# Kernel optimization log

Hardware: AMD Instinct MI355X
Metric: run time of the kernel (lower is better)

Reference implementation:

```python
import jax, jax.numpy as jnp
import numpy as np
from jax import lax

N_BLOCKS = 5
POOL = 15
N_HEADS = 8
LATENT = 32
N_EXPERTS = 4


def setup_inputs() -> dict:
    key = jax.random.key(0)
    ks = jax.random.split(key, 24)
    B, T, D = 4, 2048, 512
    H = 2 * D  # expert_dim
    s = 0.02
    f = lambda k, shp: (jax.random.normal(k, shp, jnp.float32) * s)
    return {
        'x': jax.random.normal(ks[0], (B, T, D), jnp.float32),
        # TemporalGating gate_proj
        'tg_w': f(ks[1], (D, N_BLOCKS)), 'tg_b': jnp.zeros((N_BLOCKS,), jnp.float32),
        # DualScaleFusion
        'mp_w': f(ks[2], (D, D)), 'mp_b': jnp.zeros((D,), jnp.float32),
        'fu_w': f(ks[3], (2 * D, D)), 'fu_b': jnp.zeros((D,), jnp.float32),
        # MLAAttention (all no-bias)
        'wc': f(ks[4], (D, LATENT)), 'wk': f(ks[5], (LATENT, D)),
        'wv': f(ks[6], (LATENT, D)), 'wq': f(ks[7], (D, D)), 'wo': f(ks[8], (D, D)),
        # RMSNorms
        's1': jnp.ones((D,), jnp.float32), 's2': jnp.ones((D,), jnp.float32),
        # GatedMoE
        'wr': f(ks[9], (D, N_EXPERTS)), 'br': jnp.zeros((N_EXPERTS,), jnp.float32),
        'wg': f(ks[10], (D, D)), 'bg': jnp.zeros((D,), jnp.float32),
        'w1': f(ks[11], (N_EXPERTS, D, H)), 'b1': jnp.zeros((N_EXPERTS, H), jnp.float32),
        'w2': f(ks[12], (N_EXPERTS, H, D)), 'b2': jnp.zeros((N_EXPERTS, D), jnp.float32),
    }


def _temporal_gate(x, tg_w, tg_b):
    B, T, D = x.shape
    bs = T // N_BLOCKS
    tl = N_BLOCKS * bs
    r = x[:, :tl].reshape(B, N_BLOCKS, bs, D)          # [B,nb,bs,D]
    bm = r.mean(axis=2)                                 # [B,nb,D]
    imp = jax.nn.softmax(bm @ tg_w + tg_b, axis=-1)     # [B,nb,nb]
    imp = imp.mean(axis=-1, keepdims=True)              # [B,nb,1]
    g = (r * imp[..., None]).reshape(B, tl, D)
    return jnp.pad(g, ((0, 0), (0, T - tl), (0, 0)))


def _dual_scale(x, mp_w, mp_b, fu_w, fu_b):
    # AveragePooling1D(pool=15, stride=1, SAME): TF excludes padding from the mean.
    B, T, D = x.shape
    sums = lax.reduce_window(x, 0.0, lax.add, (1, POOL, 1), (1, 1, 1), 'SAME')
    cnt = lax.reduce_window(jnp.ones((1, T, 1), x.dtype), 0.0, lax.add,
                            (1, POOL, 1), (1, 1, 1), 'SAME')
    macro = sums / cnt
    macro_feat = macro @ mp_w + mp_b
    return jnp.concatenate([x, macro_feat], axis=-1) @ fu_w + fu_b


def _mla_attn(x, wc, wk, wv, wq, wo):
    B, T, D = x.shape
    dh = D // N_HEADS
    split = lambda t: t.reshape(B, T, N_HEADS, dh).transpose(0, 2, 1, 3)
    latent = x @ wc                                      # [B,T,L]
    K, V, Q = split(latent @ wk), split(latent @ wv), split(x @ wq)
    scores = jnp.einsum('bhqd,bhkd->bhqk', Q, K) / jnp.sqrt(jnp.float32(dh))
    causal = jnp.tril(jnp.ones((T, T), jnp.float32))
    scores = scores + (1.0 - causal) * -1e9
    attn = jax.nn.softmax(scores, axis=-1)
    out = jnp.einsum('bhqk,bhkd->bhqd', attn, V).transpose(0, 2, 1, 3).reshape(B, T, D)
    return out @ wo


def _rmsnorm(x, scale, eps=1e-6):
    var = jnp.mean(jnp.square(x), axis=-1, keepdims=True)
    return scale * (x * lax.rsqrt(var + eps))


def _moe(x, wr, br, wg, bg, w1, b1, w2, b2):
    w = jax.nn.softmax(x @ wr + br, axis=-1)             # [B,T,E]
    xg = x * jax.nn.sigmoid(x @ wg + bg)
    h = jax.nn.gelu(jnp.einsum('btd,edh->bteh', xg, w1) + b1, approximate=False)
    eo = jnp.einsum('bteh,ehd->bted', h, w2) + b2        # [B,T,E,D]
    return jnp.einsum('bted,bte->btd', eo, w)


def reference(x, tg_w, tg_b, mp_w, mp_b, fu_w, fu_b, wc, wk, wv, wq, wo,
              s1, s2, wr, br, wg, bg, w1, b1, w2, b2):
    xf = _temporal_gate(x, tg_w, tg_b)
    xfu = _dual_scale(xf, mp_w, mp_b, fu_w, fu_b)
    x1 = _rmsnorm(x + _mla_attn(xfu, wc, wk, wv, wq, wo), s1)
    return _rmsnorm(x1 + _moe(x1, wr, br, wg, bg, w1, b1, w2, b2), s2)
```

## Files before the change

### kernel.cpp

```cpp
#include <hip/hip_runtime.h>
#include <math.h>

#define B_   4
#define T_   2048
#define D_   512
#define TOK  (B_*T_)
#define TL_  2045
#define GATE 0.2f
#define QSCALE 0.18033688011112043f

typedef unsigned short u16;
typedef __attribute__((ext_vector_type(8))) short short8;
typedef __attribute__((ext_vector_type(4))) float f32x4;

static __device__ __forceinline__ u16 f2u(float f){
    union { float f; unsigned u; } a; a.f = f;
    unsigned r = a.u + 0x7fffu + ((a.u >> 16) & 1u);
    return (u16)(r >> 16);
}
static __device__ __forceinline__ float u2f(u16 u){
    union { unsigned u; float f; } a; a.u = ((unsigned)u) << 16;
    return a.f;
}
static __device__ __forceinline__ f32x4 mfma16(short8 a, short8 b, f32x4 c){
    return __builtin_amdgcn_mfma_f32_16x16x32_bf16(a, b, c, 0, 0, 0);
}
static __device__ __forceinline__ void glds16(const u16* g, u16* l){
    __builtin_amdgcn_global_load_lds((const __attribute__((address_space(1))) void*)g,
                                     (__attribute__((address_space(3))) void*)l, 16, 0, 0);
}

__global__ __launch_bounds__(256) void gatepool_kernel(
    const float* __restrict__ x, u16* __restrict__ xfcat)
{
    int idx = blockIdx.x*256 + threadIdx.x;
    int d = idx & 511, g = idx >> 9;
    int b = g >> 7, t0 = (g & 127) << 4;
    const float* xp = x + ((size_t)b*2048)*512 + d;
    float v[30];
    #pragma unroll
    for (int j = 0; j < 30; ++j){
        int u = t0 - 7 + j;
        v[j] = (u >= 0 && u < TL_) ? xp[(size_t)u*512] : 0.f;
    }
    float p[31]; p[0] = 0.f;
    #pragma unroll
    for (int j = 0; j < 30; ++j) p[j+1] = p[j] + v[j];
    u16* xc = xfcat + ((size_t)(b*2048 + t0))*1024 + d;
    #pragma unroll
    for (int i = 0; i < 16; ++i){
        int t = t0 + i;
        float sum = p[i+15] - p[i];
        int lo = t-7; if (lo < 0) lo = 0;
        int hi = t+7; if (hi > 2047) hi = 2047;
        xc[(size_t)i*1024]       = f2u((t < TL_) ? GATE*v[i+7] : 0.f);
        xc[(size_t)i*1024 + 512] = f2u(GATE * sum / (float)(hi - lo + 1));
    }
}

struct TJob { const float* src; u16* dst; int K, N, ldout, coloff, tiles; float scale; };
struct TJobs { TJob j[13]; int n; };

__global__ __launch_bounds__(256) void tconv_all_kernel(TJobs JJ){
    __shared__ float t[32][33];
    int idx = blockIdx.x;
    int jb = 0;
    while (jb < JJ.n - 1 && idx >= JJ.j[jb].tiles){ idx -= JJ.j[jb].tiles; ++jb; }
    TJob J = JJ.j[jb];
    int tX = J.N >> 5;
    int k0 = (idx / tX) * 32, n0 = (idx % tX) * 32;
    int tx = threadIdx.x & 31, ty = threadIdx.x >> 5;
    #pragma unroll
    for (int i = 0; i < 32; i += 8)
        t[ty+i][tx] = J.src[(size_t)(k0+ty+i)*J.N + n0+tx];
    __syncthreads();
    #pragma unroll
    for (int i = 0; i < 32; i += 8)
        J.dst[(size_t)(n0+ty+i)*J.ldout + J.coloff + k0+tx] = f2u(J.scale * t[tx][ty+i]);
}

__global__ void convert_kernel(const float* __restrict__ in, u16* __restrict__ out){
    int idx = blockIdx.x*256 + threadIdx.x;
    out[idx] = f2u(in[idx]);
}

__global__ __launch_bounds__(256) void biasfold_kernel(
    const float* __restrict__ fu_b, const float* __restrict__ mp_b,
    const float* __restrict__ fu_w, float* __restrict__ out)
{
    int n = blockIdx.x, tid = threadIdx.x;
    float s = mp_b[tid]*fu_w[(size_t)(512+tid)*512 + n]
            + mp_b[tid+256]*fu_w[(size_t)(768+tid)*512 + n];
    for (int off = 32; off; off >>= 1) s += __shfl_down(s, off);
    __shared__ float ws[4];
    if ((tid & 63) == 0) ws[tid >> 6] = s;
    __syncthreads();
    if (tid == 0) out[n] = fu_b[n] + ws[0]+ws[1]+ws[2]+ws[3];
}

__global__ __launch_bounds__(256) void sgemm_kernel(const float* __restrict__ A,
    const float* __restrict__ B, u16* __restrict__ dstT, float* __restrict__ outF, int K){
    __shared__ float As[16][65];
    __shared__ float Bs[16][65];
    int tid = threadIdx.x;
    int tx = tid & 15, ty = tid >> 4;
    int m0 = blockIdx.y*64, n0 = blockIdx.x*64;
    int arow = tid >> 2, akq = (tid & 3) * 4;
    int bk = tid >> 4, bn = (tid & 15) * 4;
    float acc[4][4] = {};
    for (int k0 = 0; k0 < K; k0 += 16){
        const float* Ap = A + (size_t)(m0+arow)*K + k0 + akq;
        As[akq+0][arow]=Ap[0]; As[akq+1][arow]=Ap[1];
        As[akq+2][arow]=Ap[2]; As[akq+3][arow]=Ap[3];
        const float* Bp = B + (size_t)(k0+bk)*512 + n0 + bn;
        Bs[bk][bn+0]=Bp[0]; Bs[bk][bn+1]=Bp[1];
        Bs[bk][bn+2]=Bp[2]; Bs[bk][bn+3]=Bp[3];
        __syncthreads();
        #pragma unroll
        for (int kk = 0; kk < 16; ++kk){
            float av[4], bv[4];
            #pragma unroll
            for (int i=0;i<4;++i) av[i]=As[kk][ty*4+i];
            #pragma unroll
            for (int j=0;j<4;++j) bv[j]=Bs[kk][tx*4+j];
            #pragma unroll
            for (int i=0;i<4;++i)
                #pragma unroll
                for (int j=0;j<4;++j) acc[i][j] += av[i]*bv[j];
        }
        __syncthreads();
    }
    if (outF){
        #pragma unroll
        for (int i=0;i<4;++i)
            #pragma unroll
            for (int j=0;j<4;++j)
                outF[(size_t)(m0+ty*4+i)*512 + n0+tx*4+j] = acc[i][j];
    } else {
        #pragma unroll
        for (int i=0;i<4;++i)
            #pragma unroll
            for (int j=0;j<4;++j)
                dstT[(size_t)(n0+tx*4+j)*512 + m0+ty*4+i] = f2u(acc[i][j]);
    }
}

#define GF_GELU   1
#define GF_ACCUM  2
#define GF_RSCOL  4
#define GF_GLU    8
#define GF_F32OUT 16
#define GF_QKV    32

template<int MT>
__global__ __launch_bounds__(256) void mgemm_kernel(
    const u16* __restrict__ A, int lda, const u16* __restrict__ Bt, int ldb,
    const float* __restrict__ bias, const float* __restrict__ rs,
    const u16* __restrict__ glu, void* __restrict__ Cp, int ldc,
    u16* __restrict__ Cp2, int K, int flags)
{
    constexpr int MI = MT/32;
    __shared__ u16 As[MT*64];
    __shared__ u16 Bs[128*64];
    int tid = threadIdx.x;
    int wave = tid >> 6, lane = tid & 63;
    int n16 = lane & 15, quad = lane >> 4;
    int m0 = blockIdx.y * MT, n0 = blockIdx.x * 128;
    int wr = (wave >> 1) * (MT/2), wc = (wave & 1) * 64;

    f32x4 acc[MI][4] = {};

    for (int k0 = 0; k0 < K; k0 += 64){
        #pragma unroll
        for (int i = 0; i < MT/32; ++i){
            int s = i*256 + tid;
            int row = s >> 3, g = (s & 7) ^ (row & 7);
            glds16(A + (size_t)(m0+row)*lda + k0 + g*8, As + (size_t)s*8);
        }
        #pragma unroll
        for (int i = 0; i < 4; ++i){
            int s = i*256 + tid;
            int row = s >> 3, g = (s & 7) ^ (row & 7);
            glds16(Bt + (size_t)(n0+row)*ldb + k0 + g*8, Bs + (size_t)s*8);
        }
        __syncthreads();
        #pragma unroll
        for (int ks = 0; ks < 2; ++ks){
            short8 af[MI], bf[4];
            #pragma unroll
            for (int mi = 0; mi < MI; ++mi){
                int row = wr + mi*16 + n16;
                int g = (ks*4 + quad) ^ (row & 7);
                af[mi] = *(const short8*)&As[row*64 + g*8];
            }
            #pragma unroll
            for (int ni = 0; ni < 4; ++ni){
                int row = wc + ni*16 + n16;
                int g = (ks*4 + quad) ^ (row & 7);
                bf[ni] = *(const short8*)&Bs[row*64 + g*8];
            }
            #pragma unroll
            for (int mi = 0; mi < MI; ++mi)
                #pragma unroll
                for (int ni = 0; ni < 4; ++ni)
                    acc[mi][ni] = mfma16(af[mi], bf[ni], acc[mi][ni]);
        }
        __syncthreads();
    }

    if ((flags & GF_QKV) && n0 >= 1024){
        #pragma unroll
        for (int mi = 0; mi < MI; ++mi){
            int row0 = m0 + wr + mi*16 + quad*4;
            #pragma unroll
            for (int ni = 0; ni < 4; ++ni){
                int col = n0 + wc + ni*16 + n16 - 1024;
                ushort4 h4;
                h4.x = f2u(acc[mi][ni][0]); h4.y = f2u(acc[mi][ni][1]);
                h4.z = f2u(acc[mi][ni][2]); h4.w = f2u(acc[mi][ni][3]);
                *(ushort4*)&Cp2[(size_t)col*8192 + row0] = h4;
            }
        }
        return;
    }

    #pragma unroll
    for (int mi = 0; mi < MI; ++mi){
        #pragma unroll
        for (int reg = 0; reg < 4; ++reg){
            int row = m0 + wr + mi*16 + quad*4 + reg;
            #pragma unroll
            for (int ni = 0; ni < 4; ++ni){
                int col = n0 + wc + ni*16 + n16;
                float v = acc[mi][ni][reg];
                if (bias) v += bias[col];
                if (flags & GF_GELU)  v = 0.5f*v*(1.f + erff(v*0.70710678118f));
                if (flags & GF_GLU)   v = u2f(glu[(size_t)row*512 + col]) / (1.f + __expf(-v));
                if (flags & GF_RSCOL) v *= rs[(size_t)row*4 + (col >> 10)];
                size_t ci = (size_t)row*ldc + col;
                if (flags & GF_ACCUM)       ((float*)Cp)[ci] += v;
                else if (flags & GF_F32OUT) ((float*)Cp)[ci]  = v;
                else                        ((u16*)Cp)[ci]    = f2u(v);
            }
        }
    }
}

__global__ __launch_bounds__(256) void flash_kernel(
    const u16* __restrict__ QK,
    const u16* __restrict__ VT,
    u16* __restrict__ O)
{
    int bid = blockIdx.x;
    int qt = 15 - (bid >> 5);
    int bh = bid & 31;
    int h = bh & 7, b = bh >> 3;
    __shared__ u16 Ks[64*64];
    __shared__ u16 Vt[64*64];
    __shared__ u16 Ps[4][32*64];
    int tid = threadIdx.x;
    int wave = tid >> 6, lane = tid & 63;
    int n16 = lane & 15, quad = lane >> 4;
    size_t btok = (size_t)b*2048;
    size_t tok0 = btok + qt*128;

    short8 qf[2][2];
    #pragma unroll
    for (int g = 0; g < 2; ++g)
        #pragma unroll
        for (int ks = 0; ks < 2; ++ks)
            qf[g][ks] = *(const short8*)&QK[(tok0 + wave*32 + g*16 + n16)*1024
                                           + h*64 + ks*32 + quad*8];

    int qlo[2];  qlo[0] = qt*128 + wave*32; qlo[1] = qlo[0] + 16;
    int qrow[2]; qrow[0] = qlo[0] + n16;    qrow[1] = qlo[1] + n16;
    float m_st[2] = {-3.0e38f, -3.0e38f}, l_st[2] = {0.f, 0.f};
    f32x4 ov[2][4] = {};

    int nkt = 2*qt + 2;
    for (int kt = 0; kt < nkt; ++kt){
        __syncthreads();
        {
            int r = tid >> 2;
            int g0 = (tid & 3) * 2;
            const uint4* kp = (const uint4*)&QK[(btok + kt*64 + r)*1024 + 512 + h*64 + g0*8];
            uint4 ka = kp[0], kb = kp[1];
            *(uint4*)&Ks[r*64 + ((g0  ) ^ (r&7))*8] = ka;
            *(uint4*)&Ks[r*64 + ((g0+1) ^ (r&7))*8] = kb;
            const uint4* vp = (const uint4*)&VT[(size_t)(h*64 + r)*8192 + btok + kt*64 + g0*8];
            uint4 va = vp[0], vb = vp[1];
            *(uint4*)&Vt[r*64 + ((g0  ) ^ (r&7))*8] = va;
            *(uint4*)&Vt[r*64 + ((g0+1) ^ (r&7))*8] = vb;
        }
        __syncthreads();

        bool act[2];
        #pragma unroll
        for (int g = 0; g < 2; ++g){
            act[g] = (kt*64 <= qlo[g] + 15);
            if (!act[g]) continue;
            f32x4 st[4];
            #pragma unroll
            for (int ct = 0; ct < 4; ++ct){
                f32x4 a = {};
                #pragma unroll
                for (int ks = 0; ks < 2; ++ks){
                    short8 kf = *(const short8*)&Ks[(ct*16+n16)*64 + (((ks*4+quad) ^ (n16&7))*8)];
                    a = mfma16(kf, qf[g][ks], a);
                }
                st[ct] = a;
            }
            if (kt*64 + 63 > qlo[g]){
                #pragma unroll
                for (int ct = 0; ct < 4; ++ct){
                    int kb0 = kt*64 + ct*16 + quad*4;
                    #pragma unroll
                    for (int r = 0; r < 4; ++r)
                        if (kb0 + r > qrow[g]) st[ct][r] = -3.0e38f;
                }
            }
            float mx = fmaxf(fmaxf(fmaxf(st[0][0],st[0][1]),fmaxf(st[0][2],st[0][3])),
                       fmaxf(fmaxf(fmaxf(st[1][0],st[1][1]),fmaxf(st[1][2],st[1][3])),
                       fmaxf(fmaxf(fmaxf(st[2][0],st[2][1]),fmaxf(st[2][2],st[2][3])),
                             fmaxf(fmaxf(st[3][0],st[3][1]),fmaxf(st[3][2],st[3][3])))));
            mx = fmaxf(mx, __shfl_xor(mx, 16));
            mx = fmaxf(mx, __shfl_xor(mx, 32));
            float mn = fmaxf(m_st[g], mx);
            float al = exp2f(m_st[g] - mn);
            m_st[g] = mn;
            float sum = 0.f;
            #pragma unroll
            for (int ct = 0; ct < 4; ++ct)
                #pragma unroll
                for (int r = 0; r < 4; ++r){
                    float p = exp2f(st[ct][r] - mn);
                    st[ct][r] = p; sum += p;
                }
            sum += __shfl_xor(sum, 16);
            sum += __shfl_xor(sum, 32);
            l_st[g] = l_st[g]*al + sum;
            int qr = g*16 + n16;
            #pragma unroll
            for (int ct = 0; ct < 4; ++ct){
                ushort4 h4;
                h4.x = f2u(st[ct][0]); h4.y = f2u(st[ct][1]);
                h4.z = f2u(st[ct][2]); h4.w = f2u(st[ct][3]);
                int goff = ct*2 + (quad >> 1);
                *(ushort4*)&Ps[wave][qr*64 + ((goff ^ (qr&7))*8) + (quad&1)*4] = h4;
            }
            #pragma unroll
            for (int r = 0; r < 4; ++r){
                float aa = __shfl(al, quad*4 + r);
                #pragma unroll
                for (int dt = 0; dt < 4; ++dt) ov[g][dt][r] *= aa;
            }
        }
        #pragma unroll
        for (int g = 0; g < 2; ++g){
            if (!act[g]) continue;
            short8 ap[2];
            int row = g*16 + n16;
            #pragma unroll
            for (int ks = 0; ks < 2; ++ks)
                ap[ks] = *(const short8*)&Ps[wave][row*64 + (((ks*4+quad) ^ (row&7))*8)];
            #pragma unroll
            for (int dt = 0; dt < 4; ++dt)
                #pragma unroll
                for (int ks = 0; ks < 2; ++ks){
                    short8 bv = *(const short8*)&Vt[(dt*16+n16)*64 + (((ks*4+quad) ^ (n16&7))*8)];
                    ov[g][dt] = mfma16(ap[ks], bv, ov[g][dt]);
                }
        }
    }
    #pragma unroll
    for (int g = 0; g < 2; ++g)
        #pragma unroll
        for (int r = 0; r < 4; ++r){
            float li = __shfl(l_st[g], quad*4 + r);
            float inv = 1.f / li;
            size_t row = tok0 + wave*32 + g*16 + quad*4 + r;
            #pragma unroll
            for (int dt = 0; dt < 4; ++dt)
                O[row*512 + h*64 + dt*16 + n16] = f2u(ov[g][dt][r] * inv);
        }
}

__global__ __launch_bounds__(256) void rmsnorm_kernel(
    const float* __restrict__ x, const u16* __restrict__ y,
    const float* __restrict__ scale, u16* __restrict__ out)
{
    int tok = blockIdx.x, tid = threadIdx.x;
    size_t base = (size_t)tok * 512;
    float v0 = x[base+tid]     + u2f(y[base+tid]);
    float v1 = x[base+tid+256] + u2f(y[base+tid+256]);
    float ss = v0*v0 + v1*v1;
    for (int off = 32; off; off >>= 1) ss += __shfl_down(ss, off);
    __shared__ float ws[4];
    if ((tid & 63) == 0) ws[tid >> 6] = ss;
    __syncthreads();
    float rstd = rsqrtf((ws[0]+ws[1]+ws[2]+ws[3])*(1.f/512.f) + 1e-6f);
    out[base+tid]     = f2u(scale[tid]     * v0 * rstd);
    out[base+tid+256] = f2u(scale[tid+256] * v1 * rstd);
}

__global__ __launch_bounds__(256) void final_kernel(
    const u16* __restrict__ x1, const float* __restrict__ moe,
    const float* __restrict__ rout, const float* __restrict__ b2,
    const float* __restrict__ scale, float* __restrict__ out)
{
    int tok = blockIdx.x, tid = threadIdx.x;
    size_t base = (size_t)tok * 512;
    float r0 = rout[tok*4+0], r1 = rout[tok*4+1], r2 = rout[tok*4+2], r3 = rout[tok*4+3];
    float bb0 = r0*b2[tid]     + r1*b2[512+tid]     + r2*b2[1024+tid]     + r3*b2[1536+tid];
    float bb1 = r0*b2[tid+256] + r1*b2[768+tid]     + r2*b2[1280+tid]     + r3*b2[1792+tid];
    float v0 = u2f(x1[base+tid])     + moe[base+tid]     + bb0;
    float v1 = u2f(x1[base+tid+256]) + moe[base+tid+256] + bb1;
    float ss = v0*v0 + v1*v1;
    for (int off = 32; off; off >>= 1) ss += __shfl_down(ss, off);
    __shared__ float ws[4];
    if ((tid & 63) == 0) ws[tid >> 6] = ss;
    __syncthreads();
    float rstd = rsqrtf((ws[0]+ws[1]+ws[2]+ws[3])*(1.f/512.f) + 1e-6f);
    out[base+tid]     = scale[tid]     * v0 * rstd;
    out[base+tid+256] = scale[tid+256] * v1 * rstd;
}

__global__ __launch_bounds__(256) void router_kernel(
    const u16* __restrict__ x1, const float* __restrict__ wr,
    const float* __restrict__ br, float* __restrict__ rout)
{
    int wid = threadIdx.x >> 6, lane = threadIdx.x & 63;
    int tok = blockIdx.x*4 + wid;
    const u16* xp = x1 + (size_t)tok*512;
    float p0=0.f, p1=0.f, p2=0.f, p3=0.f;
    for (int d = lane; d < 512; d += 64){
        float xv = u2f(xp[d]);
        p0 += xv*wr[d*4+0]; p1 += xv*wr[d*4+1];
        p2 += xv*wr[d*4+2]; p3 += xv*wr[d*4+3];
    }
    for (int off = 32; off; off >>= 1){
        p0 += __shfl_down(p0,off); p1 += __shfl_down(p1,off);
        p2 += __shfl_down(p2,off); p3 += __shfl_down(p3,off);
    }
    if (lane == 0){
        p0 += br[0]; p1 += br[1]; p2 += br[2]; p3 += br[3];
        float mx = fmaxf(fmaxf(p0,p1), fmaxf(p2,p3));
        float e0=__expf(p0-mx), e1=__expf(p1-mx), e2=__expf(p2-mx), e3=__expf(p3-mx);
        float inv = 1.f/(e0+e1+e2+e3);
        rout[tok*4+0]=e0*inv; rout[tok*4+1]=e1*inv;
        rout[tok*4+2]=e2*inv; rout[tok*4+3]=e3*inv;
    }
}

extern "C" void kernel_launch(void* const* d_in, const int* in_sizes, int n_in,
                              void* d_out, int out_size, void* d_ws, size_t ws_size,
                              hipStream_t stream)
{
    const float* x    = (const float*)d_in[0];
    const float* mp_w = (const float*)d_in[3];
    const float* mp_b = (const float*)d_in[4];
    const float* fu_w = (const float*)d_in[5];
    const float* fu_b = (const float*)d_in[6];
    const float* wc   = (const float*)d_in[7];
    const float* wk   = (const float*)d_in[8];
    const float* wv   = (const float*)d_in[9];
    const float* wq   = (const float*)d_in[10];
    const float* wo   = (const float*)d_in[11];
    const float* s1   = (const float*)d_in[12];
    const float* s2   = (const float*)d_in[13];
    const float* wr   = (const float*)d_in[14];
    const float* br   = (const float*)d_in[15];
    const float* wg   = (const float*)d_in[16];
    const float* bg   = (const float*)d_in[17];
    const float* w1   = (const float*)d_in[18];
    const float* b1   = (const float*)d_in[19];
    const float* w2   = (const float*)d_in[20];
    const float* b2   = (const float*)d_in[21];

    char* wsb = (char*)d_ws;
    const size_t MB = 1024*1024;
    const size_t KB512 = 512*1024;
    u16*   wqkvT  = (u16*)(wsb + 0);
    u16*   woT    = (u16*)(wsb + 3*KB512);
    u16*   wgT    = (u16*)(wsb + 4*KB512);
    u16*   WfuT2  = (u16*)(wsb + 5*KB512);
    u16*   fuBT   = (u16*)(wsb + 7*KB512);
    u16*   mp_wB  = (u16*)(wsb + 8*KB512);
    u16*   w1T    = (u16*)(wsb + 9*KB512);
    u16*   w2Ts   = (u16*)(wsb + 17*KB512);
    float* WcvF   = (float*)(wsb + 25*KB512);
    float* fubias = (float*)(wsb + 27*KB512);
    float* ROUT   = (float*)(wsb + 27*KB512 + 4096);
    u16*   XFcat = (u16*)(wsb + 14*MB);
    float* MOE   = (float*)(wsb + 14*MB);
    u16*   S3    = (u16*)(wsb + 14*MB);
    u16*   XFU   = (u16*)(wsb + 30*MB);
    u16*   XG    = (u16*)(wsb + 30*MB);
    u16*   QKb   = (u16*)(wsb + 38*MB);
    u16*   Hb    = (u16*)(wsb + 38*MB);
    u16*   ATT   = (u16*)(wsb + 54*MB);
    u16*   VbT   = (u16*)(wsb + 70*MB);
    u16*   x1h   = (u16*)(wsb + 78*MB);

    auto mg128 = [&](const u16* A, int lda, const u16* Bt, int ldb, const float* bias,
                     const float* rs, const u16* glu, void* C, int ldc, u16* C2,
                     int M, int N, int K, int flags){
        dim3 g(N/128, M/128);
        mgemm_kernel<128><<<g, 256, 0, stream>>>(A, lda, Bt, ldb, bias, rs, glu, C, ldc, C2, K, flags);
    };
    auto mg64 = [&](const u16* A, int lda, const u16* Bt, int ldb, const float* bias,
                    const float* rs, const u16* glu, void* C, int ldc, u16* C2,
                    int M, int N, int K, int flags){
        dim3 g(N/128, M/64);
        mgemm_kernel<64><<<g, 256, 0, stream>>>(A, lda, Bt, ldb, bias, rs, glu, C, ldc, C2, K, flags);
    };

    TJobs JJ; JJ.n = 13;
    auto setj = [&](int i, const float* src, u16* dst, int K, int N, int ldout,
                    int coloff, float scale){
        JJ.j[i] = TJob{src, dst, K, N, ldout, coloff, (K/32)*(N/32), scale};
    };
    setj(0, wq,            wqkvT, 512,  512,  512, 0, QSCALE);
    setj(1, wo,            woT,   512,  512,  512, 0, 1.f);
    setj(2, wg,            wgT,   512,  512,  512, 0, 1.f);
    setj(3, fu_w,          WfuT2, 512,  512, 1024, 0, 1.f);
    setj(4, fu_w + 512*512,fuBT,  512,  512,  512, 0, 1.f);
    for (int e = 0; e < 4; ++e){
        setj(5+e, w1 + (size_t)e*512*1024, w1T + (size_t)e*1024*512, 512, 1024, 512, 0, 1.f);
        setj(9+e, w2 + (size_t)e*1024*512, w2Ts + (size_t)e*1024, 1024, 512, 4096, 0, 1.f);
    }
    int nt = 5*256 + 4*512 + 4*512;
    tconv_all_kernel<<<nt, 256, 0, stream>>>(JJ);
    convert_kernel<<<512*512/256, 256, 0, stream>>>(mp_w, mp_wB);
    sgemm_kernel<<<dim3(8,8), 256, 0, stream>>>(wc, wk, wqkvT + 512*512, nullptr, 32);
    sgemm_kernel<<<dim3(8,8), 256, 0, stream>>>(wc, wv, wqkvT + 1024*512, nullptr, 32);
    biasfold_kernel<<<512, 256, 0, stream>>>(fu_b, mp_b, fu_w, fubias);
    mg64(fuBT, 512, mp_wB, 512, 0, 0, 0, WfuT2 + 512, 1024, 0, 512, 512, 512, 0);
    (void)WcvF;

    gatepool_kernel<<<(TOK/16)*512/256, 256, 0, stream>>>(x, XFcat);
    mg64 (XFcat, 1024, WfuT2, 1024, fubias, 0, 0, XFU, 512, 0, TOK, 512, 1024, 0);
    mg64 (XFU, 512, wqkvT, 512, 0, 0, 0, QKb, 1024, VbT, TOK, 1536, 512, GF_QKV);
    flash_kernel<<<512, 256, 0, stream>>>(QKb, VbT, ATT);
    mg64 (ATT, 512, woT, 512, 0, 0, 0, S3, 512, 0, TOK, 512, 512, 0);
    rmsnorm_kernel<<<TOK, 256, 0, stream>>>(x, S3, s1, x1h);
    router_kernel<<<TOK/4, 256, 0, stream>>>(x1h, wr, br, ROUT);
    mg64 (x1h, 512, wgT, 512, bg, 0, x1h, XG, 512, 0, TOK, 512, 512, GF_GLU);
    for (int p = 0; p < 2; ++p){
        mg128(XG, 512, w1T + (size_t)p*2048*512, 512, b1 + p*2048, ROUT + p*2, 0,
              Hb, 2048, 0, TOK, 2048, 512, GF_GELU | GF_RSCOL);
        mg64 (Hb, 2048, w2Ts + p*2048, 4096, 0, 0, 0,
              MOE, 512, 0, TOK, 512, 2048, p ? GF_ACCUM : GF_F32OUT);
    }
    final_kernel<<<TOK, 256, 0, stream>>>(x1h, MOE, ROUT, b2, s2, (float*)d_out);
}
```

Before: 588.2 us.

## Fold fusion GEMM into QKV weights and split MoE by token halves

Measured after the change: 612.9 us. +4.2%, slower.

```diff
diff --git a/kernel.cpp b/kernel.cpp
--- a/kernel.cpp
+++ b/kernel.cpp
@@ -98,8 +98,22 @@
     if (tid == 0) out[n] = fu_b[n] + ws[0]+ws[1]+ws[2]+ws[3];
 }
 
+__global__ __launch_bounds__(256) void qkvbias_kernel(
+    const float* __restrict__ fubias, const u16* __restrict__ wqkvT,
+    float* __restrict__ out)
+{
+    int n = blockIdx.x, tid = threadIdx.x;
+    const u16* wp = wqkvT + (size_t)n*512;
+    float s = fubias[tid]*u2f(wp[tid]) + fubias[tid+256]*u2f(wp[tid+256]);
+    for (int off = 32; off; off >>= 1) s += __shfl_down(s, off);
+    __shared__ float ws[4];
+    if ((tid & 63) == 0) ws[tid >> 6] = s;
+    __syncthreads();
+    if (tid == 0) out[n] = ws[0]+ws[1]+ws[2]+ws[3];
+}
+
 __global__ __launch_bounds__(256) void sgemm_kernel(const float* __restrict__ A,
-    const float* __restrict__ B, u16* __restrict__ dstT, float* __restrict__ outF, int K){
+    const float* __restrict__ B, u16* __restrict__ dstT, int K){
     __shared__ float As[16][65];
     __shared__ float Bs[16][65];
     int tid = threadIdx.x;
@@ -130,26 +144,16 @@
         }
         __syncthreads();
     }
-    if (outF){
-        #pragma unroll
-        for (int i=0;i<4;++i)
-            #pragma unroll
-            for (int j=0;j<4;++j)
-                outF[(size_t)(m0+ty*4+i)*512 + n0+tx*4+j] = acc[i][j];
-    } else {
-        #pragma unroll
-        for (int i=0;i<4;++i)
-            #pragma unroll
-            for (int j=0;j<4;++j)
-                dstT[(size_t)(n0+tx*4+j)*512 + m0+ty*4+i] = f2u(acc[i][j]);
-    }
+    #pragma unroll
+    for (int i=0;i<4;++i)
+        #pragma unroll
+        for (int j=0;j<4;++j)
+            dstT[(size_t)(n0+tx*4+j)*512 + m0+ty*4+i] = f2u(acc[i][j]);
 }
 
 #define GF_GELU   1
-#define GF_ACCUM  2
 #define GF_RSCOL  4
 #define GF_GLU    8
-#define GF_F32OUT 16
 #define GF_QKV    32
 
 template<int MT>
@@ -214,11 +218,12 @@
             int row0 = m0 + wr + mi*16 + quad*4;
             #pragma unroll
             for (int ni = 0; ni < 4; ++ni){
-                int col = n0 + wc + ni*16 + n16 - 1024;
+                int col = n0 + wc + ni*16 + n16;
+                float bb = bias[col];
                 ushort4 h4;
-                h4.x = f2u(acc[mi][ni][0]); h4.y = f2u(acc[mi][ni][1]);
-                h4.z = f2u(acc[mi][ni][2]); h4.w = f2u(acc[mi][ni][3]);
-                *(ushort4*)&Cp2[(size_t)col*8192 + row0] = h4;
+                h4.x = f2u(acc[mi][ni][0] + bb); h4.y = f2u(acc[mi][ni][1] + bb);
+                h4.z = f2u(acc[mi][ni][2] + bb); h4.w = f2u(acc[mi][ni][3] + bb);
+                *(ushort4*)&Cp2[(size_t)(col-1024)*8192 + row0] = h4;
             }
         }
         return;
@@ -237,10 +242,7 @@
                 if (flags & GF_GELU)  v = 0.5f*v*(1.f + erff(v*0.70710678118f));
                 if (flags & GF_GLU)   v = u2f(glu[(size_t)row*512 + col]) / (1.f + __expf(-v));
                 if (flags & GF_RSCOL) v *= rs[(size_t)row*4 + (col >> 10)];
-                size_t ci = (size_t)row*ldc + col;
-                if (flags & GF_ACCUM)       ((float*)Cp)[ci] += v;
-                else if (flags & GF_F32OUT) ((float*)Cp)[ci]  = v;
-                else                        ((u16*)Cp)[ci]    = f2u(v);
+                ((u16*)Cp)[(size_t)row*ldc + col] = f2u(v);
             }
         }
     }
@@ -404,7 +406,7 @@
 }
 
 __global__ __launch_bounds__(256) void final_kernel(
-    const u16* __restrict__ x1, const float* __restrict__ moe,
+    const u16* __restrict__ x1, const u16* __restrict__ moe,
     const float* __restrict__ rout, const float* __restrict__ b2,
     const float* __restrict__ scale, float* __restrict__ out)
 {
@@ -413,8 +415,8 @@
     float r0 = rout[tok*4+0], r1 = rout[tok*4+1], r2 = rout[tok*4+2], r3 = rout[tok*4+3];
     float bb0 = r0*b2[tid]     + r1*b2[512+tid]     + r2*b2[1024+tid]     + r3*b2[1536+tid];
     float bb1 = r0*b2[tid+256] + r1*b2[768+tid]     + r2*b2[1280+tid]     + r3*b2[1792+tid];
-    float v0 = u2f(x1[base+tid])     + moe[base+tid]     + bb0;
-    float v1 = u2f(x1[base+tid+256]) + moe[base+tid+256] + bb1;
+    float v0 = u2f(x1[base+tid])     + u2f(moe[base+tid])     + bb0;
+    float v1 = u2f(x1[base+tid+256]) + u2f(moe[base+tid+256]) + bb1;
     float ss = v0*v0 + v1*v1;
     for (int off = 32; off; off >>= 1) ss += __shfl_down(ss, off);
     __shared__ float ws[4];
@@ -479,28 +481,27 @@
 
     char* wsb = (char*)d_ws;
     const size_t MB = 1024*1024;
-    const size_t KB512 = 512*1024;
-    u16*   wqkvT  = (u16*)(wsb + 0);
-    u16*   woT    = (u16*)(wsb + 3*KB512);
-    u16*   wgT    = (u16*)(wsb + 4*KB512);
-    u16*   WfuT2  = (u16*)(wsb + 5*KB512);
-    u16*   fuBT   = (u16*)(wsb + 7*KB512);
-    u16*   mp_wB  = (u16*)(wsb + 8*KB512);
-    u16*   w1T    = (u16*)(wsb + 9*KB512);
-    u16*   w2Ts   = (u16*)(wsb + 17*KB512);
-    float* WcvF   = (float*)(wsb + 25*KB512);
-    float* fubias = (float*)(wsb + 27*KB512);
-    float* ROUT   = (float*)(wsb + 27*KB512 + 4096);
-    u16*   XFcat = (u16*)(wsb + 14*MB);
-    float* MOE   = (float*)(wsb + 14*MB);
-    u16*   S3    = (u16*)(wsb + 14*MB);
-    u16*   XFU   = (u16*)(wsb + 30*MB);
-    u16*   XG    = (u16*)(wsb + 30*MB);
-    u16*   QKb   = (u16*)(wsb + 38*MB);
-    u16*   Hb    = (u16*)(wsb + 38*MB);
-    u16*   ATT   = (u16*)(wsb + 54*MB);
-    u16*   VbT   = (u16*)(wsb + 70*MB);
-    u16*   x1h   = (u16*)(wsb + 78*MB);
+    u16*   WqkvC  = (u16*)(wsb + 0);
+    u16*   woT    = (u16*)(wsb + 3*MB);
+    u16*   wgT    = (u16*)(wsb + 3*MB + 512*1024);
+    u16*   w1T    = (u16*)(wsb + 4*MB);
+    u16*   w2Ts   = (u16*)(wsb + 8*MB);
+    float* fubias = (float*)(wsb + 12*MB);
+    float* qkvbias= (float*)(wsb + 12*MB + 4096);
+    float* ROUT   = (float*)(wsb + 12*MB + 16384);
+    u16*   wqkvT  = (u16*)(wsb + 25*MB/2);
+    u16*   fuBT   = (u16*)(wsb + 14*MB);
+    u16*   mp_wB  = (u16*)(wsb + 29*MB/2);
+    u16*   WfuBF  = (u16*)(wsb + 15*MB);
+    u16*   XFcat = (u16*)(wsb + 16*MB);
+    u16*   S3    = (u16*)(wsb + 16*MB);
+    u16*   MOE   = (u16*)(wsb + 16*MB);
+    u16*   x1h   = (u16*)(wsb + 24*MB);
+    u16*   QKb   = (u16*)(wsb + 32*MB);
+    u16*   XG    = (u16*)(wsb + 32*MB);
+    u16*   Hb    = (u16*)(wsb + 40*MB);
+    u16*   VbT   = (u16*)(wsb + 48*MB);
+    u16*   ATT   = (u16*)(wsb + 56*MB);
 
     auto mg128 = [&](const u16* A, int lda, const u16* Bt, int ldb, const float* bias,
                      const float* rs, const u16* glu, void* C, int ldc, u16* C2,
@@ -515,7 +516,7 @@
         mgemm_kernel<64><<<g, 256, 0, stream>>>(A, lda, Bt, ldb, bias, rs, glu, C, ldc, C2, K, flags);
     };
 
-    TJobs JJ; JJ.n = 13;
+    TJobs JJ; JJ.n = 11;
     auto setj = [&](int i, const float* src, u16* dst, int K, int N, int ldout,
                     int coloff, float scale){
         JJ.j[i] = TJob{src, dst, K, N, ldout, coloff, (K/32)*(N/32), scale};
@@ -523,34 +524,34 @@
     setj(0, wq,            wqkvT, 512,  512,  512, 0, QSCALE);
     setj(1, wo,            woT,   512,  512,  512, 0, 1.f);
     setj(2, wg,            wgT,   512,  512,  512, 0, 1.f);
-    setj(3, fu_w,          WfuT2, 512,  512, 1024, 0, 1.f);
-    setj(4, fu_w + 512*512,fuBT,  512,  512,  512, 0, 1.f);
+    setj(3, fu_w + 512*512,fuBT,  512,  512,  512, 0, 1.f);
     for (int e = 0; e < 4; ++e){
-        setj(5+e, w1 + (size_t)e*512*1024, w1T + (size_t)e*1024*512, 512, 1024, 512, 0, 1.f);
-        setj(9+e, w2 + (size_t)e*1024*512, w2Ts + (size_t)e*1024, 1024, 512, 4096, 0, 1.f);
-    }
-    int nt = 5*256 + 4*512 + 4*512;
+        setj(4+e, w1 + (size_t)e*512*1024, w1T + (size_t)e*1024*512, 512, 1024, 512, 0, 1.f);
+        setj(8+e, w2 + (size_t)e*1024*512, w2Ts + (size_t)e*1024, 1024, 512, 4096, 0, 1.f);
+    }
+    int nt = 4*256 + 8*512;
     tconv_all_kernel<<<nt, 256, 0, stream>>>(JJ);
     convert_kernel<<<512*512/256, 256, 0, stream>>>(mp_w, mp_wB);
-    sgemm_kernel<<<dim3(8,8), 256, 0, stream>>>(wc, wk, wqkvT + 512*512, nullptr, 32);
-    sgemm_kernel<<<dim3(8,8), 256, 0, stream>>>(wc, wv, wqkvT + 1024*512, nullptr, 32);
+    convert_kernel<<<512*512/256, 256, 0, stream>>>(fu_w, WfuBF);
+    sgemm_kernel<<<dim3(8,8), 256, 0, stream>>>(wc, wk, wqkvT + 512*512, 32);
+    sgemm_kernel<<<dim3(8,8), 256, 0, stream>>>(wc, wv, wqkvT + 1024*512, 32);
     biasfold_kernel<<<512, 256, 0, stream>>>(fu_b, mp_b, fu_w, fubias);
-    mg64(fuBT, 512, mp_wB, 512, 0, 0, 0, WfuT2 + 512, 1024, 0, 512, 512, 512, 0);
-    (void)WcvF;
+    qkvbias_kernel<<<1536, 256, 0, stream>>>(fubias, wqkvT, qkvbias);
+    mg64(mp_wB, 512, fuBT, 512, 0, 0, 0, WfuBF + 512*512, 512, 0, 512, 512, 512, 0);
+    mg64(wqkvT, 512, WfuBF, 512, 0, 0, 0, WqkvC, 1024, 0, 1536, 1024, 512, 0);
 
     gatepool_kernel<<<(TOK/16)*512/256, 256, 0, stream>>>(x, XFcat);
-    mg64 (XFcat, 1024, WfuT2, 1024, fubias, 0, 0, XFU, 512, 0, TOK, 512, 1024, 0);
-    mg64 (XFU, 512, wqkvT, 512, 0, 0, 0, QKb, 1024, VbT, TOK, 1536, 512, GF_QKV);
+    mg64 (XFcat, 1024, WqkvC, 1024, qkvbias, 0, 0, QKb, 1024, VbT, TOK, 1536, 1024, GF_QKV);
     flash_kernel<<<512, 256, 0, stream>>>(QKb, VbT, ATT);
     mg64 (ATT, 512, woT, 512, 0, 0, 0, S3, 512, 0, TOK, 512, 512, 0);
     rmsnorm_kernel<<<TOK, 256, 0, stream>>>(x, S3, s1, x1h);
     router_kernel<<<TOK/4, 256, 0, stream>>>(x1h, wr, br, ROUT);
     mg64 (x1h, 512, wgT, 512, bg, 0, x1h, XG, 512, 0, TOK, 512, 512, GF_GLU);
-    for (int p = 0; p < 2; ++p){
-        mg128(XG, 512, w1T + (size_t)p*2048*512, 512, b1 + p*2048, ROUT + p*2, 0,
-              Hb, 2048, 0, TOK, 2048, 512, GF_GELU | GF_RSCOL);
-        mg64 (Hb, 2048, w2Ts + p*2048, 4096, 0, 0, 0,
-              MOE, 512, 0, TOK, 512, 2048, p ? GF_ACCUM : GF_F32OUT);
+    for (int h = 0; h < 2; ++h){
+        mg128(XG + (size_t)h*4096*512, 512, w1T, 512, b1, ROUT + (size_t)h*4096*4, 0,
+              Hb, 4096, 0, 4096, 4096, 512, GF_GELU | GF_RSCOL);
+        mg64 (Hb, 4096, w2Ts, 4096, 0, 0, 0,
+              MOE + (size_t)h*4096*512, 512, 0, 4096, 512, 4096, 0);
     }
     final_kernel<<<TOK, 256, 0, stream>>>(x1h, MOE, ROUT, b2, s2, (float*)d_out);
 }
```
